# Kernel tuning notes

Hardware: AMD Instinct MI355X
Metric: run time of the kernel (lower is better)

Reference implementation:

```python
import jax, jax.numpy as jnp
import numpy as np

K, STRIDE, PAD, DIL = 3, 1, 1, 1


def setup_inputs() -> dict:
    key = jax.random.key(0)
    k0, k1, k2, k3, k4 = jax.random.split(key, 5)
    B, Cin, Cout, H, W = 16, 64, 64, 64, 64
    x = jax.random.normal(k0, (B, Cin, H, W), dtype=jnp.float32)
    # NOTE: the torch module zero-inits conv_offset; we use small random
    # weights so the deformable sampling path is actually exercised.
    w_off = jax.random.normal(k1, (2 * K * K, Cin, K, K), dtype=jnp.float32) * 0.01
    b_off = jax.random.normal(k2, (2 * K * K,), dtype=jnp.float32) * 0.01
    fan_in = Cin * K * K
    w_dcn = jax.random.normal(k3, (Cout, Cin, K, K), dtype=jnp.float32) / np.sqrt(fan_in)
    b_dcn = jax.random.normal(k4, (Cout,), dtype=jnp.float32) * 0.01
    return {"x": x, "w_off": w_off, "b_off": b_off, "w_dcn": w_dcn, "b_dcn": b_dcn}


def _conv2d(x, w, b, stride, pad):
    out = jax.lax.conv_general_dilated(
        x, w, window_strides=(stride, stride), padding=[(pad, pad), (pad, pad)],
        dimension_numbers=("NCHW", "OIHW", "NCHW"))
    return out + b[None, :, None, None]


def _deform_conv(x, offset, w, b, stride, pad, dil):
    # torchvision-style DeformConv2d, groups=1, no modulation mask.
    B, Cin, H, W = x.shape
    Cout = w.shape[0]
    Ho = (H + 2 * pad - dil * (K - 1) - 1) // stride + 1
    Wo = (W + 2 * pad - dil * (K - 1) - 1) // stride + 1
    KK = K * K
    # base sampling grid: p0 + dilation*kernel_tap + learned offset
    oy = (jnp.arange(Ho) * stride - pad).astype(x.dtype)
    ox = (jnp.arange(Wo) * stride - pad).astype(x.dtype)
    ky, kx = jnp.meshgrid(jnp.arange(K), jnp.arange(K), indexing="ij")
    ky = (ky * dil).reshape(-1).astype(x.dtype)  # [KK], row (y) of tap
    kx = (kx * dil).reshape(-1).astype(x.dtype)
    # offset channel layout: [y_0, x_0, y_1, x_1, ...] -> [B, KK, 2, Ho, Wo]
    off = offset.reshape(B, KK, 2, Ho, Wo)
    py = off[:, :, 0] + ky[None, :, None, None] + oy[None, None, :, None]  # [B,KK,Ho,Wo]
    px = off[:, :, 1] + kx[None, :, None, None] + ox[None, None, None, :]
    y0 = jnp.floor(py)
    x0 = jnp.floor(px)
    wy1 = py - y0
    wx1 = px - x0
    wy0 = 1.0 - wy1
    wx0 = 1.0 - wx1
    x_flat = x.reshape(B, Cin, H * W)

    def gather(yi, xi):
        valid = (yi >= 0) & (yi < H) & (xi >= 0) & (xi < W)  # zero padding outside
        yc = jnp.clip(yi, 0, H - 1).astype(jnp.int32)
        xc = jnp.clip(xi, 0, W - 1).astype(jnp.int32)
        idx = (yc * W + xc).reshape(B, 1, -1)
        v = jnp.take_along_axis(x_flat, idx, axis=2).reshape(B, Cin, KK, Ho, Wo)
        return v * valid.astype(x.dtype).reshape(B, 1, KK, Ho, Wo)

    cols = (gather(y0, x0) * (wy0 * wx0)[:, None]
            + gather(y0, x0 + 1) * (wy0 * wx1)[:, None]
            + gather(y0 + 1, x0) * (wy1 * wx0)[:, None]
            + gather(y0 + 1, x0 + 1) * (wy1 * wx1)[:, None])  # [B,Cin,KK,Ho,Wo]
    out = jnp.einsum("bckhw,ock->bohw", cols, w.reshape(Cout, Cin, KK))
    return out + b[None, :, None, None]


def reference(x, w_off, b_off, w_dcn, b_dcn):
    offset = _conv2d(x, w_off, b_off, STRIDE, PAD)
    return _deform_conv(x, offset, w_dcn, b_dcn, STRIDE, PAD, DIL)
```

## Files before the change

kernel.cpp:

```cpp
#include <hip/hip_runtime.h>
#include <hip/hip_fp16.h>


#define KOFF 18
#define CPAD 72
#define GSTR 33

#define W2T_HALFS    (18 * 64 * 32)
#define WOFF2T_HALFS (18 * 32 * 32)
#define W2T_BYTES    (W2T_HALFS * 2)
#define WOFF2T_OFF   W2T_BYTES
#define X_OFF        (W2T_BYTES + WOFF2T_HALFS * 2)
#define XH_BYTES     (16 * 64 * 64 * 64 * 2)
#define WS_NEED      (X_OFF + XH_BYTES)

typedef _Float16 half8 __attribute__((ext_vector_type(8)));
typedef float floatx4 __attribute__((ext_vector_type(4)));

union H8 { half8 v; __half2 h2[4]; uint4 u; };

__global__ void prep(const float* __restrict__ x,
                     const float* __restrict__ w_dcn,
                     const float* __restrict__ w_off,
                     _Float16* __restrict__ w2t,
                     _Float16* __restrict__ woff2t,
                     _Float16* __restrict__ xh) {
    int e = blockIdx.x * 256 + threadIdx.x;
    {
        int xx = e & 63, y = (e >> 6) & 63, cin = (e >> 12) & 63, b = e >> 18;
        xh[((((size_t)b * 64 + y) * 64 + xx) << 6) + cin] = (_Float16)x[e];
    }
    if (e < W2T_HALFS) {
        int kl = e & 31, co = (e >> 5) & 63, i = e >> 11;
        int tap = i >> 1, cin = (i & 1) * 32 + kl;
        w2t[e] = (_Float16)w_dcn[co * 576 + cin * 9 + tap];
    } else if (e < W2T_HALFS + WOFF2T_HALFS) {
        int e2 = e - W2T_HALFS;
        int kl = e2 & 31, co = (e2 >> 5) & 31, i = e2 >> 10;
        int tap = i >> 1, cin = (i & 1) * 32 + kl;
        woff2t[e2] = (co < KOFF) ? (_Float16)w_off[co * 576 + cin * 9 + tap]
                                 : (_Float16)0.f;
    }
}

__launch_bounds__(256, 4)
__global__ void dcn_main(const _Float16* __restrict__ xh,
                         const _Float16* __restrict__ w2t,
                         const _Float16* __restrict__ woff2t,
                         const float* __restrict__ b_off,
                         const float* __restrict__ b_dcn,
                         float* __restrict__ out) {
    const int bid = blockIdx.x;
    const int s   = bid >> 3;
    const int b   = ((bid & 7) << 1) | (s >> 7);
    const int ho  = (s >> 1) & 63;
    const int hlf = s & 1;
    const int t    = threadIdx.x;
    const int lane = t & 63;
    const int wid  = __builtin_amdgcn_readfirstlane(t >> 6);
    const int r    = lane & 15;
    const int q    = lane >> 4;
    const int gpx  = t >> 3;
    const int oct  = t & 7;
    const int pxg  = hlf * 32;

    __shared__ __align__(16) _Float16 colsT[2][32 * CPAD];
    __shared__ __align__(16) float    offlds[KOFF * 32];
    __shared__ __align__(16) uint4    grecL[9 * GSTR];

    const _Float16* xb = xh + ((size_t)b << 18);
    const char* xpb = (const char*)xb;

    {
        floatx4 am = {0.f, 0.f, 0.f, 0.f};
        const int m = wid & 1, n = wid >> 1;

        auto stageA = [&](int tap) {
            const int dy = tap / 3, dxk = tap - dy * 3;
            const int y  = ho + dy - 1;
            const int xc = pxg + gpx + dxk - 1;
            half8 v = {};
            if (((unsigned)y < 64u) && ((unsigned)xc < 64u))
                v = *(const half8*)&xb[(((size_t)y * 64 + xc) << 6) + oct * 8];
            *(half8*)&colsT[tap & 1][gpx * CPAD + oct * 8] = v;
        };

        stageA(0);
        __syncthreads();
#pragma unroll
        for (int tap = 0; tap < 9; ++tap) {
            if (tap < 8) stageA(tap + 1);
#pragma unroll
            for (int g = 0; g < 2; ++g) {
                half8 a = *(const half8*)&woff2t[(tap * 2 + g) * 1024
                                                 + (m * 16 + r) * 32 + q * 8];
                half8 bf = *(const half8*)&colsT[tap & 1][(n * 16 + r) * CPAD
                                                          + g * 32 + q * 8];
                am = __builtin_amdgcn_mfma_f32_16x16x32_f16(a, bf, am, 0, 0, 0);
            }
            __syncthreads();
        }
#pragma unroll
        for (int reg = 0; reg < 4; ++reg) {
            int co = m * 16 + q * 4 + reg;
            if (co < KOFF)
                offlds[co * 32 + n * 16 + r] = am[reg] + b_off[co];
        }
    }
    __syncthreads();

    for (int e = t; e < 9 * 32; e += 256) {
        int tap = e >> 5, px = e & 31;
        float offy = offlds[(2 * tap) * 32 + px];
        float offx = offlds[(2 * tap + 1) * 32 + px];
        float py  = offy + (float)(tap / 3) + (float)(ho - 1);
        float pxf = offx + (float)(tap % 3) + (float)(pxg + px - 1);
        float fy = floorf(py), fx = floorf(pxf);
        int y0 = (int)fy, x0 = (int)fx;
        float wy1 = py - fy, wx1 = pxf - fx;
        float wy0 = 1.f - wy1, wx0 = 1.f - wx1;
        bool y0ok = ((unsigned)y0 < 64u);
        bool x0ok = ((unsigned)x0 < 64u);
        bool y1ok = ((unsigned)(y0 + 1) < 64u);
        bool x1ok = ((unsigned)(x0 + 1) < 64u);
        float w00 = (y0ok && x0ok) ? wy0 * wx0 : 0.f;
        float w01 = (y0ok && x1ok) ? wy0 * wx1 : 0.f;
        float w10 = (y1ok && x0ok) ? wy1 * wx0 : 0.f;
        float w11 = (y1ok && x1ok) ? wy1 * wx1 : 0.f;
        int yc0 = min(max(y0, 0), 63);
        int xc0 = min(max(x0, 0), 63);
        int yc1 = min(max(y0 + 1, 0), 63);
        int xc1 = min(max(x0 + 1, 0), 63);
        union { __half2 h; unsigned u; } c0, c1;
        c0.h = __floats2half2_rn(w00, w01);
        c1.h = __floats2half2_rn(w10, w11);
        uint4 rec;
        rec.x = (unsigned)(yc0 * 64 + xc0)
              | ((unsigned)(xc1 - xc0) << 12)
              | ((unsigned)(yc1 - yc0) << 13);
        rec.y = c0.u;
        rec.z = c1.u;
        rec.w = 0u;
        grecL[tap * GSTR + px] = rec;
    }
    __syncthreads();

    floatx4 acc0 = {0.f, 0.f, 0.f, 0.f};
    floatx4 acc1 = {0.f, 0.f, 0.f, 0.f};

    auto gather = [&](int tap) {
        uint4 rec = grecL[tap * GSTR + gpx];
        unsigned a00 = (rec.x & 0xfffu) * 128u + (unsigned)oct * 16u;
        unsigned dx128  = ((rec.x >> 12) & 1u) * 128u;
        unsigned dy8192 = ((rec.x >> 13) & 1u) * 8192u;
        unsigned a01 = a00 + dx128;
        unsigned a10 = a00 + dy8192;
        unsigned a11 = a10 + dx128;
        H8 v00, v01, v10, v11;
        v00.v = *(const half8*)(xpb + a00);
        v01.v = *(const half8*)(xpb + a01);
        v10.v = *(const half8*)(xpb + a10);
        v11.v = *(const half8*)(xpb + a11);
        union { unsigned u; __half2 h; } cy, cz;
        cy.u = rec.y; cz.u = rec.z;
        __half2 W00 = __half2half2(__low2half(cy.h));
        __half2 W01 = __half2half2(__high2half(cy.h));
        __half2 W10 = __half2half2(__low2half(cz.h));
        __half2 W11 = __half2half2(__high2half(cz.h));
        H8 res;
#pragma unroll
        for (int c = 0; c < 4; ++c) {
            __half2 aa = __hmul2(v00.h2[c], W00);
            aa = __hfma2(v01.h2[c], W01, aa);
            aa = __hfma2(v10.h2[c], W10, aa);
            aa = __hfma2(v11.h2[c], W11, aa);
            res.h2[c] = aa;
        }
        *(half8*)&colsT[tap & 1][gpx * CPAD + oct * 8] = res.v;
    };

    gather(0);
    __syncthreads();
#pragma unroll
    for (int tap = 0; tap < 9; ++tap) {
        if (tap < 8) gather(tap + 1);
#pragma unroll
        for (int g = 0; g < 2; ++g) {
            half8 af = *(const half8*)&w2t[(size_t)(tap * 2 + g) * 2048
                                           + (wid * 16 + r) * 32 + q * 8];
            half8 b0 = *(const half8*)&colsT[tap & 1][r * CPAD + g * 32 + q * 8];
            half8 b1 = *(const half8*)&colsT[tap & 1][(16 + r) * CPAD + g * 32 + q * 8];
            acc0 = __builtin_amdgcn_mfma_f32_16x16x32_f16(af, b0, acc0, 0, 0, 0);
            acc1 = __builtin_amdgcn_mfma_f32_16x16x32_f16(af, b1, acc1, 0, 0, 0);
        }
        if (tap < 8) __syncthreads();
    }

#pragma unroll
    for (int reg = 0; reg < 4; ++reg) {
        int co = wid * 16 + q * 4 + reg;
        float bias = b_dcn[co];
        size_t o = (((size_t)b * 64 + co) * 64 + ho) * 64 + pxg;
        out[o + r]      = acc0[reg] + bias;
        out[o + 16 + r] = acc1[reg] + bias;
    }
}

#define FCPAD 40
__launch_bounds__(256, 4)
__global__ void dcn_fb(const float* __restrict__ x,
                       const float* __restrict__ w_dcn,
                       const float* __restrict__ w_off,
                       const float* __restrict__ b_off,
                       const float* __restrict__ b_dcn,
                       float* __restrict__ out) {
    const int bid = blockIdx.x;
    const int s   = bid >> 3;
    const int b   = ((bid & 7) << 1) | (s >> 7);
    const int ho  = (s >> 1) & 63;
    const int hlf = s & 1;
    const int t    = threadIdx.x;
    const int lane = t & 63;
    const int wid  = __builtin_amdgcn_readfirstlane(t >> 6);
    const int r    = lane & 15;
    const int q    = lane >> 4;
    const int px   = t & 31;
    const int kq   = t >> 5;

    __shared__ __align__(16) _Float16 colsT[2][32 * FCPAD];
    __shared__ __align__(16) float    offlds[KOFF * 32];

    const float* xb = x + (size_t)b * 64 * 4096;
    const int pxg = hlf * 32;

    {
        floatx4 am = {0.f, 0.f, 0.f, 0.f};
        const int m = wid & 1, n = wid >> 1;
        auto stageA = [&](int i) {
            const int tap = i >> 1;
            const int dy = tap / 3, dxk = tap - dy * 3;
            const int y  = ho + dy - 1;
            const int xc = pxg + px + dxk - 1;
            const bool ok = ((unsigned)y < 64u) && ((unsigned)xc < 64u);
            const float* xp = xb + ((size_t)((i & 1) * 32 + kq * 4)) * 4096
                                 + y * 64 + xc;
            float va[4];
#pragma unroll
            for (int j = 0; j < 4; ++j) va[j] = ok ? xp[(size_t)j * 4096] : 0.f;
#pragma unroll
            for (int j = 0; j < 4; ++j)
                colsT[i & 1][px * FCPAD + kq * 4 + j] = (_Float16)va[j];
        };
        auto loadA = [&](int i) -> half8 {
            const int tap = i >> 1;
            const int cin0 = (i & 1) * 32 + q * 8;
            const int co = m * 16 + r;
            half8 v;
#pragma unroll
            for (int j = 0; j < 8; ++j)
                v[j] = (co < KOFF) ? (_Float16)w_off[co * 576 + (cin0 + j) * 9 + tap]
                                   : (_Float16)0.f;
            return v;
        };
        stageA(0);
        __syncthreads();
#pragma unroll
        for (int i = 0; i < 18; ++i) {
            if (i < 17) stageA(i + 1);
            half8 a = loadA(i);
            half8 bfr = *(const half8*)&colsT[i & 1][(n * 16 + r) * FCPAD + q * 8];
            am = __builtin_amdgcn_mfma_f32_16x16x32_f16(a, bfr, am, 0, 0, 0);
            __syncthreads();
        }
#pragma unroll
        for (int reg = 0; reg < 4; ++reg) {
            int co = m * 16 + q * 4 + reg;
            if (co < KOFF)
                offlds[co * 32 + (n * 16 + r)] = am[reg] + b_off[co];
        }
    }
    __syncthreads();

    unsigned rmeta[9], rw0[9], rw1[9];
#pragma unroll
    for (int tap = 0; tap < 9; ++tap) {
        float offy = offlds[(2 * tap) * 32 + px];
        float offx = offlds[(2 * tap + 1) * 32 + px];
        float py  = offy + (float)(tap / 3) + (float)(ho - 1);
        float pxf = offx + (float)(tap % 3) + (float)(pxg + px - 1);
        float fy = floorf(py), fx = floorf(pxf);
        int y0 = (int)fy, x0 = (int)fx;
        float wy1 = py - fy, wx1 = pxf - fx;
        float wy0 = 1.f - wy1, wx0 = 1.f - wx1;
        bool y0ok = ((unsigned)y0 < 64u);
        bool x0ok = ((unsigned)x0 < 64u);
        bool y1ok = ((unsigned)(y0 + 1) < 64u);
        bool x1ok = ((unsigned)(x0 + 1) < 64u);
        float w00 = (y0ok && x0ok) ? wy0 * wx0 : 0.f;
        float w01 = (y0ok && x1ok) ? wy0 * wx1 : 0.f;
        float w10 = (y1ok && x0ok) ? wy1 * wx0 : 0.f;
        float w11 = (y1ok && x1ok) ? wy1 * wx1 : 0.f;
        int yc0 = min(max(y0, 0), 63);
        int xc0 = min(max(x0, 0), 63);
        int yc1 = min(max(y0 + 1, 0), 63);
        int xc1 = min(max(x0 + 1, 0), 63);
        union { __half2 h; unsigned u; } c0, c1;
        c0.h = __floats2half2_rn(w00, w01);
        c1.h = __floats2half2_rn(w10, w11);
        rmeta[tap] = (unsigned)(yc0 * 64 + xc0)
                   | ((unsigned)(xc1 - xc0) << 12)
                   | ((unsigned)(yc1 - yc0) << 13);
        rw0[tap] = c0.u;
        rw1[tap] = c1.u;
    }

    floatx4 acc0 = {0.f, 0.f, 0.f, 0.f};
    floatx4 acc1 = {0.f, 0.f, 0.f, 0.f};

    auto gather = [&](int i) {
        const int tap = i >> 1;
        const unsigned m = rmeta[tap];
        const unsigned a00 = (m & 0xfffu) << 2;
        const unsigned a01 = a00 + ((m >> 10) & 4u);
        const unsigned a10 = a00 + ((m >> 5) & 256u);
        const unsigned a11 = a10 + ((m >> 10) & 4u);
        const char* base = (const char*)xb
                         + ((size_t)((i & 1) * 32 + kq * 4)) * 16384;
        float v00[4], v01[4], v10[4], v11[4];
#pragma unroll
        for (int j = 0; j < 4; ++j) {
            const char* xp = base + (size_t)j * 16384;
            v00[j] = *(const float*)(xp + a00);
            v01[j] = *(const float*)(xp + a01);
            v10[j] = *(const float*)(xp + a10);
            v11[j] = *(const float*)(xp + a11);
        }
        union { unsigned u; __half2 h; } c0, c1;
        c0.u = rw0[tap]; c1.u = rw1[tap];
        const float wA = __half2float(c0.h.x), wB = __half2float(c0.h.y);
        const float wC = __half2float(c1.h.x), wD = __half2float(c1.h.y);
#pragma unroll
        for (int j = 0; j < 4; ++j)
            colsT[i & 1][px * FCPAD + kq * 4 + j] =
                (_Float16)(v00[j] * wA + v01[j] * wB + v10[j] * wC + v11[j] * wD);
    };

    auto load_af = [&](int i) -> half8 {
        const int tap = i >> 1;
        const int cin0 = (i & 1) * 32 + q * 8;
        half8 v;
#pragma unroll
        for (int j = 0; j < 8; ++j)
            v[j] = (_Float16)w_dcn[(wid * 16 + r) * 576 + (cin0 + j) * 9 + tap];
        return v;
    };

    gather(0);
    __syncthreads();
#pragma unroll
    for (int i = 0; i < 18; ++i) {
        if (i < 17) gather(i + 1);
        half8 af = load_af(i);
        half8 b0 = *(const half8*)&colsT[i & 1][r * FCPAD + q * 8];
        half8 b1 = *(const half8*)&colsT[i & 1][(16 + r) * FCPAD + q * 8];
        acc0 = __builtin_amdgcn_mfma_f32_16x16x32_f16(af, b0, acc0, 0, 0, 0);
        acc1 = __builtin_amdgcn_mfma_f32_16x16x32_f16(af, b1, acc1, 0, 0, 0);
        if (i < 17) __syncthreads();
    }

#pragma unroll
    for (int reg = 0; reg < 4; ++reg) {
        int co = wid * 16 + q * 4 + reg;
        float bias = b_dcn[co];
        size_t o = (((size_t)b * 64 + co) * 64 + ho) * 64 + pxg;
        out[o + r]      = acc0[reg] + bias;
        out[o + 16 + r] = acc1[reg] + bias;
    }
}

extern "C" void kernel_launch(void* const* d_in, const int* in_sizes, int n_in,
                              void* d_out, int out_size, void* d_ws, size_t ws_size,
                              hipStream_t stream) {
    const float* x     = (const float*)d_in[0];
    const float* w_off = (const float*)d_in[1];
    const float* b_off = (const float*)d_in[2];
    const float* w_dcn = (const float*)d_in[3];
    const float* b_dcn = (const float*)d_in[4];
    float* out = (float*)d_out;

    char* ws = (char*)d_ws;
    _Float16* w2t    = (_Float16*)ws;
    _Float16* woff2t = (_Float16*)(ws + WOFF2T_OFF);
    _Float16* xh     = (_Float16*)(ws + X_OFF);

    if (ws_size >= (size_t)WS_NEED) {
        prep<<<16384, 256, 0, stream>>>(x, w_dcn, w_off, w2t, woff2t, xh);
        dcn_main<<<2048, 256, 0, stream>>>(xh, w2t, woff2t, b_off, b_dcn, out);
    } else {
        dcn_fb<<<2048, 256, 0, stream>>>(x, w_dcn, w_off, b_off, b_dcn, out);
    }
}
```

Measured before the change: 123.5 us.

## Software-pipeline gathers and weight loads; tile NCHW→NHWC transpose via LDS

The prep kernel now transposes x to NHWC fp16 through a shared-memory tile per (batch,row), so both global reads and writes are coalesced instead of doing scattered 2-byte writes. The launch shrinks to 1240 blocks. In both MFMA loops of dcn_main, the global loads for the next tap (input gathers and weight fragments) are issued into registers before the current tap's MFMAs. Their results are written to LDS afterwards, so memory latency overlaps with matrix math. This raises register pressure, which could affect occupancy under the 256x4 launch bounds.

Result: faster. 110.2 us (-10.8%).

```diff
diff --git a/kernel.cpp b/kernel.cpp
--- a/kernel.cpp
+++ b/kernel.cpp
@@ -25,21 +25,42 @@
                      _Float16* __restrict__ w2t,
                      _Float16* __restrict__ woff2t,
                      _Float16* __restrict__ xh) {
-    int e = blockIdx.x * 256 + threadIdx.x;
-    {
-        int xx = e & 63, y = (e >> 6) & 63, cin = (e >> 12) & 63, b = e >> 18;
-        xh[((((size_t)b * 64 + y) * 64 + xx) << 6) + cin] = (_Float16)x[e];
-    }
-    if (e < W2T_HALFS) {
-        int kl = e & 31, co = (e >> 5) & 63, i = e >> 11;
-        int tap = i >> 1, cin = (i & 1) * 32 + kl;
-        w2t[e] = (_Float16)w_dcn[co * 576 + cin * 9 + tap];
-    } else if (e < W2T_HALFS + WOFF2T_HALFS) {
-        int e2 = e - W2T_HALFS;
-        int kl = e2 & 31, co = (e2 >> 5) & 31, i = e2 >> 10;
-        int tap = i >> 1, cin = (i & 1) * 32 + kl;
-        woff2t[e2] = (co < KOFF) ? (_Float16)w_off[co * 576 + cin * 9 + tap]
-                                 : (_Float16)0.f;
+    const int bi = blockIdx.x;
+    const int t  = threadIdx.x;
+    if (bi < 1024) {
+        const int b = bi >> 6, y = bi & 63;
+        __shared__ __align__(16) _Float16 tile[64 * CPAD];
+        const int xx = t & 63;
+        const int c4 = t >> 6;
+        const float* xp = x + (((size_t)b * 64) * 64 + y) * 64;
+#pragma unroll
+        for (int p = 0; p < 16; ++p) {
+            int cin = p * 4 + c4;
+            tile[xx * CPAD + cin] = (_Float16)xp[(size_t)cin * 4096 + xx];
+        }
+        __syncthreads();
+        const int oct = t & 7;
+        const int xl  = t >> 3;
+        _Float16* op = xh + ((((size_t)b * 64 + y) * 64) << 6);
+#pragma unroll
+        for (int p = 0; p < 2; ++p) {
+            int xr = p * 32 + xl;
+            half8 v = *(const half8*)&tile[xr * CPAD + oct * 8];
+            *(half8*)&op[(size_t)xr * 64 + oct * 8] = v;
+        }
+    } else {
+        int e = (bi - 1024) * 256 + t;
+        if (e < W2T_HALFS) {
+            int kl = e & 31, co = (e >> 5) & 63, i = e >> 11;
+            int tap = i >> 1, cin = (i & 1) * 32 + kl;
+            w2t[e] = (_Float16)w_dcn[co * 576 + cin * 9 + tap];
+        } else {
+            int e2 = e - W2T_HALFS;
+            int kl = e2 & 31, co = (e2 >> 5) & 31, i = e2 >> 10;
+            int tap = i >> 1, cin = (i & 1) * 32 + kl;
+            woff2t[e2] = (co < KOFF) ? (_Float16)w_off[co * 576 + cin * 9 + tap]
+                                     : (_Float16)0.f;
+        }
     }
 }
 
@@ -75,28 +96,39 @@
         floatx4 am = {0.f, 0.f, 0.f, 0.f};
         const int m = wid & 1, n = wid >> 1;
 
-        auto stageA = [&](int tap) {
+        auto loadS = [&](int tap) -> half8 {
             const int dy = tap / 3, dxk = tap - dy * 3;
             const int y  = ho + dy - 1;
             const int xc = pxg + gpx + dxk - 1;
             half8 v = {};
             if (((unsigned)y < 64u) && ((unsigned)xc < 64u))
                 v = *(const half8*)&xb[(((size_t)y * 64 + xc) << 6) + oct * 8];
-            *(half8*)&colsT[tap & 1][gpx * CPAD + oct * 8] = v;
+            return v;
         };
-
-        stageA(0);
+        auto loadWA = [&](int tap, int g) -> half8 {
+            return *(const half8*)&woff2t[(tap * 2 + g) * 1024
+                                          + (m * 16 + r) * 32 + q * 8];
+        };
+
+        half8 sv = loadS(0);
+        *(half8*)&colsT[0][gpx * CPAD + oct * 8] = sv;
+        half8 a0 = loadWA(0, 0), a1 = loadWA(0, 1);
         __syncthreads();
 #pragma unroll
         for (int tap = 0; tap < 9; ++tap) {
-            if (tap < 8) stageA(tap + 1);
-#pragma unroll
-            for (int g = 0; g < 2; ++g) {
-                half8 a = *(const half8*)&woff2t[(tap * 2 + g) * 1024
-                                                 + (m * 16 + r) * 32 + q * 8];
-                half8 bf = *(const half8*)&colsT[tap & 1][(n * 16 + r) * CPAD
-                                                          + g * 32 + q * 8];
-                am = __builtin_amdgcn_mfma_f32_16x16x32_f16(a, bf, am, 0, 0, 0);
+            half8 sn, a0n, a1n;
+            if (tap < 8) {
+                sn  = loadS(tap + 1);
+                a0n = loadWA(tap + 1, 0);
+                a1n = loadWA(tap + 1, 1);
+            }
+            half8 bf0 = *(const half8*)&colsT[tap & 1][(n * 16 + r) * CPAD + q * 8];
+            half8 bf1 = *(const half8*)&colsT[tap & 1][(n * 16 + r) * CPAD + 32 + q * 8];
+            am = __builtin_amdgcn_mfma_f32_16x16x32_f16(a0, bf0, am, 0, 0, 0);
+            am = __builtin_amdgcn_mfma_f32_16x16x32_f16(a1, bf1, am, 0, 0, 0);
+            if (tap < 8) {
+                *(half8*)&colsT[(tap + 1) & 1][gpx * CPAD + oct * 8] = sn;
+                a0 = a0n; a1 = a1n;
             }
             __syncthreads();
         }
@@ -148,21 +180,24 @@
     floatx4 acc0 = {0.f, 0.f, 0.f, 0.f};
     floatx4 acc1 = {0.f, 0.f, 0.f, 0.f};
 
-    auto gather = [&](int tap) {
+    struct G { H8 a, c, d, e; unsigned wy, wz; };
+
+    auto loadB = [&](int tap) -> G {
         uint4 rec = grecL[tap * GSTR + gpx];
         unsigned a00 = (rec.x & 0xfffu) * 128u + (unsigned)oct * 16u;
         unsigned dx128  = ((rec.x >> 12) & 1u) * 128u;
         unsigned dy8192 = ((rec.x >> 13) & 1u) * 8192u;
-        unsigned a01 = a00 + dx128;
-        unsigned a10 = a00 + dy8192;
-        unsigned a11 = a10 + dx128;
-        H8 v00, v01, v10, v11;
-        v00.v = *(const half8*)(xpb + a00);
-        v01.v = *(const half8*)(xpb + a01);
-        v10.v = *(const half8*)(xpb + a10);
-        v11.v = *(const half8*)(xpb + a11);
+        G g;
+        g.a.v = *(const half8*)(xpb + a00);
+        g.c.v = *(const half8*)(xpb + a00 + dx128);
+        g.d.v = *(const half8*)(xpb + a00 + dy8192);
+        g.e.v = *(const half8*)(xpb + a00 + dy8192 + dx128);
+        g.wy = rec.y; g.wz = rec.z;
+        return g;
+    };
+    auto storeB = [&](int tap, G& g) {
         union { unsigned u; __half2 h; } cy, cz;
-        cy.u = rec.y; cz.u = rec.z;
+        cy.u = g.wy; cz.u = g.wz;
         __half2 W00 = __half2half2(__low2half(cy.h));
         __half2 W01 = __half2half2(__high2half(cy.h));
         __half2 W10 = __half2half2(__low2half(cz.h));
@@ -170,30 +205,47 @@
         H8 res;
 #pragma unroll
         for (int c = 0; c < 4; ++c) {
-            __half2 aa = __hmul2(v00.h2[c], W00);
-            aa = __hfma2(v01.h2[c], W01, aa);
-            aa = __hfma2(v10.h2[c], W10, aa);
-            aa = __hfma2(v11.h2[c], W11, aa);
+            __half2 aa = __hmul2(g.a.h2[c], W00);
+            aa = __hfma2(g.c.h2[c], W01, aa);
+            aa = __hfma2(g.d.h2[c], W10, aa);
+            aa = __hfma2(g.e.h2[c], W11, aa);
             res.h2[c] = aa;
         }
         *(half8*)&colsT[tap & 1][gpx * CPAD + oct * 8] = res.v;
     };
-
-    gather(0);
+    auto loadW = [&](int tap, int g) -> half8 {
+        return *(const half8*)&w2t[(size_t)(tap * 2 + g) * 2048
+                                   + (wid * 16 + r) * 32 + q * 8];
+    };
+
+    {
+        G g0 = loadB(0);
+        storeB(0, g0);
+    }
+    half8 af0 = loadW(0, 0), af1 = loadW(0, 1);
     __syncthreads();
 #pragma unroll
     for (int tap = 0; tap < 9; ++tap) {
-        if (tap < 8) gather(tap + 1);
-#pragma unroll
-        for (int g = 0; g < 2; ++g) {
-            half8 af = *(const half8*)&w2t[(size_t)(tap * 2 + g) * 2048
-                                           + (wid * 16 + r) * 32 + q * 8];
-            half8 b0 = *(const half8*)&colsT[tap & 1][r * CPAD + g * 32 + q * 8];
-            half8 b1 = *(const half8*)&colsT[tap & 1][(16 + r) * CPAD + g * 32 + q * 8];
-            acc0 = __builtin_amdgcn_mfma_f32_16x16x32_f16(af, b0, acc0, 0, 0, 0);
-            acc1 = __builtin_amdgcn_mfma_f32_16x16x32_f16(af, b1, acc1, 0, 0, 0);
-        }
-        if (tap < 8) __syncthreads();
+        G gn;
+        half8 af0n, af1n;
+        if (tap < 8) {
+            gn   = loadB(tap + 1);
+            af0n = loadW(tap + 1, 0);
+            af1n = loadW(tap + 1, 1);
+        }
+        half8 b00 = *(const half8*)&colsT[tap & 1][r * CPAD + q * 8];
+        half8 b10 = *(const half8*)&colsT[tap & 1][(16 + r) * CPAD + q * 8];
+        half8 b01 = *(const half8*)&colsT[tap & 1][r * CPAD + 32 + q * 8];
+        half8 b11 = *(const half8*)&colsT[tap & 1][(16 + r) * CPAD + 32 + q * 8];
+        acc0 = __builtin_amdgcn_mfma_f32_16x16x32_f16(af0, b00, acc0, 0, 0, 0);
+        acc1 = __builtin_amdgcn_mfma_f32_16x16x32_f16(af0, b10, acc1, 0, 0, 0);
+        acc0 = __builtin_amdgcn_mfma_f32_16x16x32_f16(af1, b01, acc0, 0, 0, 0);
+        acc1 = __builtin_amdgcn_mfma_f32_16x16x32_f16(af1, b11, acc1, 0, 0, 0);
+        if (tap < 8) {
+            storeB(tap + 1, gn);
+            af0 = af0n; af1 = af1n;
+            __syncthreads();
+        }
     }
 
 #pragma unroll
@@ -394,7 +446,7 @@
     _Float16* xh     = (_Float16*)(ws + X_OFF);
 
     if (ws_size >= (size_t)WS_NEED) {
-        prep<<<16384, 256, 0, stream>>>(x, w_dcn, w_off, w2t, woff2t, xh);
+        prep<<<1240, 256, 0, stream>>>(x, w_dcn, w_off, w2t, woff2t, xh);
         dcn_main<<<2048, 256, 0, stream>>>(xh, w2t, woff2t, b_off, b_dcn, out);
     } else {
         dcn_fb<<<2048, 256, 0, stream>>>(x, w_dcn, w_off, b_off, b_dcn, out);
```
